# Kernel tuning notes

Hardware: AMD Instinct MI355X
Metric: run time of the kernel (lower is better)

## Reference

```python
import jax, jax.numpy as jnp
import numpy as np

NUM_CODES = 8192
LATENT_DIM = 256
BETA = 0.25
EPS_NORM = 1e-12  # F.normalize eps


def setup_inputs() -> dict:
    key = jax.random.key(0)
    k1, k2 = jax.random.split(key)
    z = jax.random.normal(k1, (8, LATENT_DIM, 32, 32), dtype=jnp.float32)
    # embedding initialized uniform(-1/K, 1/K); use that scale for realism
    codebook = jax.random.uniform(k2, (NUM_CODES, LATENT_DIM), dtype=jnp.float32,
                                  minval=-1.0 / NUM_CODES, maxval=1.0 / NUM_CODES)
    return {"z": z, "codebook": codebook}


def reference(z, codebook):
    # forward re-normalizes the codebook rows (F.normalize dim=1)
    norm = jnp.sqrt(jnp.sum(codebook * codebook, axis=1, keepdims=True))
    w = codebook / jnp.maximum(norm, EPS_NORM)                      # [K, D]

    z_perm = jnp.transpose(z, (0, 2, 3, 1))                          # [B, H, W, D]
    B, H, W, D = z_perm.shape
    zf = z_perm.reshape(-1, D)                                       # [N, D]

    # squared euclidean distances: ||z||^2 + ||w||^2 - 2 z w^T
    d = (jnp.sum(zf * zf, axis=1, keepdims=True)
         + jnp.sum(w * w, axis=1)
         - 2.0 * jnp.einsum('nd,kd->nk', zf, w))                     # [N, K]
    idx = jnp.argmin(d, axis=1)                                      # [N] int

    z_q = w[idx].reshape(B, H, W, D)                                 # gather

    # commitment + codebook loss
    loss = (jnp.mean((jax.lax.stop_gradient(z_q) - z_perm) ** 2)
            + BETA * jnp.mean((z_q - jax.lax.stop_gradient(z_perm)) ** 2))

    # straight-through estimator
    z_q = z_perm + jax.lax.stop_gradient(z_q - z_perm)

    # perplexity from codeword usage histogram (== mean of one-hots)
    N = idx.shape[0]
    counts = jnp.zeros((NUM_CODES,), dtype=jnp.float32).at[idx].add(1.0)
    avg_probs = counts / N
    perplexity = jnp.exp(-jnp.sum(avg_probs * jnp.log(avg_probs + 1e-10)))

    z_q = jnp.transpose(z_q, (0, 3, 1, 2))                           # back to NCHW
    return (z_q, idx, loss, perplexity)
```

## Files before the change

kernel.cpp:

```cpp
#include <hip/hip_runtime.h>
#include <hip/hip_bf16.h>
#include <math.h>

#define KC 8192
#define DD 256
#define NP 8192
#define ZQ_ELEMS 2097152
#define MARGIN_S 2.5e-4f
#define NPART 8

#define OFF_ABIG 0u
#define OFF_BBIG 8388608u
#define OFF_NRM  16777216u
#define OFF_WSQ  16809984u
#define OFF_PV1  16875520u
#define OFF_PV2  17924096u
#define OFF_PK1  18972672u
#define OFF_LOSSP 20021248u
#define OFF_HIST 20090880u
#define OFF_PACK 20123648u
#define OFF_LIST 20189184u
#define OFF_NFLG 20221952u

typedef __attribute__((ext_vector_type(8))) short bf16x8;
typedef __attribute__((ext_vector_type(4))) float f32x4;
typedef __attribute__((address_space(3))) void as3_void;
typedef const __attribute__((address_space(1))) void as1_cvoid;

#define GLOAD16(g, l) __builtin_amdgcn_global_load_lds((as1_cvoid*)(g), (as3_void*)(l), 16, 0, 0)

__device__ inline double waveReduceD(double v) {
#pragma unroll
    for (int off = 32; off; off >>= 1) v += __shfl_down(v, off, 64);
    return v;
}

static __device__ inline unsigned short f2bf(float f) {
    __hip_bfloat16 h = __float2bfloat16(f);
    return *(unsigned short*)&h;
}
static __device__ inline float bf2f(unsigned short u) {
    unsigned v = ((unsigned)u) << 16;
    float f;
    __builtin_memcpy(&f, &v, 4);
    return f;
}

__global__ __launch_bounds__(256) void prep(
    const float* __restrict__ cb, const float* __restrict__ z,
    unsigned short* __restrict__ Bbig, unsigned short* __restrict__ Abig,
    float* __restrict__ nrm, float* __restrict__ wsq,
    int* __restrict__ hist, int* __restrict__ nflag) {
    int bid = blockIdx.x, t = threadIdx.x;
    int lane = t & 63, wid = t >> 6;
    if (bid < 2048) {
        if (bid < 32) hist[bid * 256 + t] = 0;
        if (bid == 32 && t == 0) *nflag = 0;
        int k = bid * 4 + wid;
        float4 c4 = *(const float4*)&cb[(size_t)k * DD + lane * 4];
        double s = (double)c4.x * c4.x + (double)c4.y * c4.y
                 + (double)c4.z * c4.z + (double)c4.w * c4.w;
#pragma unroll
        for (int off = 32; off; off >>= 1) s += __shfl_xor(s, off, 64);
        float mh = fmaxf(sqrtf((float)s), 1e-12f);
        if (lane == 0) {
            nrm[k] = mh;
            wsq[k] = (float)(s / ((double)mh * (double)mh));
        }
        float wv[4] = {c4.x / mh, c4.y / mh, c4.z / mh, c4.w / mh};
        unsigned short hi[4], lo[4];
#pragma unroll
        for (int j = 0; j < 4; ++j) {
            hi[j] = f2bf(wv[j]);
            lo[j] = f2bf(wv[j] - bf2f(hi[j]));
        }
        *(ushort4*)&Bbig[(size_t)k * 512 + lane * 4] = make_ushort4(hi[0], hi[1], hi[2], hi[3]);
        *(ushort4*)&Bbig[(size_t)k * 512 + 256 + lane * 4] = make_ushort4(lo[0], lo[1], lo[2], lo[3]);
    } else {
        __shared__ float tile[64][65];
        int zb = bid - 2048;
        int b = zb >> 6, ht = (zb >> 2) & 15, dt = zb & 3;
        int hw0 = ht * 64, d0 = dt * 64;
#pragma unroll
        for (int i = 0; i < 16; ++i) {
            int dl = wid * 16 + i;
            tile[dl][lane] = z[(size_t)(b * DD + d0 + dl) * 1024 + hw0 + lane];
        }
        __syncthreads();
#pragma unroll
        for (int i = 0; i < 16; ++i) {
            int nl = wid * 16 + i;
            float v = tile[lane][nl];
            unsigned short hi = f2bf(v);
            unsigned short lo = f2bf(v - bf2f(hi));
            size_t base = (size_t)(b * 1024 + hw0 + nl) * 512 + d0 + lane;
            Abig[base] = hi;
            Abig[base + 256] = lo;
        }
    }
}

__global__ __launch_bounds__(512, 2) void gemm_top2(
    const unsigned short* __restrict__ Abig, const unsigned short* __restrict__ Bbig,
    const float* __restrict__ wsq,
    float* __restrict__ pv1, float* __restrict__ pv2, int* __restrict__ pk1) {
    __shared__ unsigned short sAB[65536];

    int t = threadIdx.x;
    int l = t & 63, w = t >> 6;
    int wm = w >> 2, wn = w & 3;
    int kc0 = blockIdx.y * 1024;
    int n0 = blockIdx.x * 256;

    int row0 = t >> 2;
    int lsw = (((t & 3) ^ ((row0 >> 1) & 3)) << 3);
    int subsw = (((l >> 4) ^ ((l >> 1) & 3)) << 3);

#define STAGE(g_) do {                                                         \
    int ct_ = (g_) / 24;                                                       \
    int kt_ = (g_) % 24;                                                       \
    int p_ = kt_ >> 3;                                                         \
    int zo_ = (p_ == 2 ? 256 : 0) + (kt_ & 7) * 32;                            \
    int wo_ = (p_ == 1 ? 256 : 0) + (kt_ & 7) * 32;                            \
    int b_ = ((g_) & 3) * 16384;                                               \
    int kc_ = kc0 + ct_ * 256;                                                 \
    GLOAD16(Bbig + (size_t)(kc_ + row0) * 512 + wo_ + lsw, &sAB[b_ + t * 8]);  \
    GLOAD16(Bbig + (size_t)(kc_ + row0 + 128) * 512 + wo_ + lsw, &sAB[b_ + 4096 + t * 8]); \
    GLOAD16(Abig + (size_t)(n0 + row0) * 512 + zo_ + lsw, &sAB[b_ + 8192 + t * 8]); \
    GLOAD16(Abig + (size_t)(n0 + row0 + 128) * 512 + zo_ + lsw, &sAB[b_ + 12288 + t * 8]); \
} while (0)

#define LDFRAG(bufbase, fa, fb) do {                                           \
    _Pragma("unroll")                                                          \
    for (int mf = 0; mf < 8; ++mf)                                             \
        fa[mf] = *(const bf16x8*)&sAB[(bufbase) + (wm * 128 + mf * 16 + (l & 15)) * 32 + subsw]; \
    _Pragma("unroll")                                                          \
    for (int nf = 0; nf < 4; ++nf)                                             \
        fb[nf] = *(const bf16x8*)&sAB[(bufbase) + 8192 + (wn * 64 + nf * 16 + (l & 15)) * 32 + subsw]; \
} while (0)

#define MFMACL(fa, fb) do {                                                    \
    __builtin_amdgcn_s_setprio(1);                                             \
    _Pragma("unroll")                                                          \
    for (int mf = 0; mf < 8; ++mf)                                             \
        _Pragma("unroll")                                                      \
        for (int nf = 0; nf < 4; ++nf)                                         \
            acc[mf][nf] = __builtin_amdgcn_mfma_f32_16x16x32_bf16(fa[mf], fb[nf], acc[mf][nf], 0, 0, 0); \
    __builtin_amdgcn_s_setprio(0);                                             \
} while (0)

#define WAITBAR(n_) do {                                                       \
    asm volatile("s_waitcnt vmcnt(" #n_ ")" ::: "memory");                     \
    __builtin_amdgcn_s_barrier();                                              \
    asm volatile("" ::: "memory");                                             \
} while (0)

#define RESETACC(ct_) do {                                                     \
    _Pragma("unroll")                                                          \
    for (int mf = 0; mf < 8; ++mf) {                                           \
        _Pragma("unroll")                                                      \
        for (int r = 0; r < 4; ++r) {                                          \
            float hv = -0.5f * wsq[kc0 + (ct_) * 256 + wm * 128 + mf * 16 + ((l >> 4) << 2) + r]; \
            _Pragma("unroll")                                                  \
            for (int nf = 0; nf < 4; ++nf) acc[mf][nf][r] = hv;                \
        }                                                                      \
    }                                                                          \
} while (0)

#define EXTRACT(ct_) do {                                                      \
    _Pragma("unroll")                                                          \
    for (int mf = 0; mf < 8; ++mf) {                                           \
        _Pragma("unroll")                                                      \
        for (int r = 0; r < 4; ++r) {                                          \
            int code = kc0 + (ct_) * 256 + wm * 128 + mf * 16 + ((l >> 4) << 2) + r; \
            _Pragma("unroll")                                                  \
            for (int nf = 0; nf < 4; ++nf) {                                   \
                float dv = -acc[mf][nf][r];                                    \
                bool lt = dv < v1[nf];                                         \
                v2[nf] = fminf(v2[nf], fmaxf(v1[nf], dv));                     \
                v1[nf] = fminf(v1[nf], dv);                                    \
                k1[nf] = lt ? code : k1[nf];                                   \
            }                                                                  \
        }                                                                      \
    }                                                                          \
} while (0)

    float v1[4], v2[4];
    int k1[4];
#pragma unroll
    for (int nf = 0; nf < 4; ++nf) { v1[nf] = 3.4e38f; v2[nf] = 3.4e38f; k1[nf] = 0; }

    f32x4 acc[8][4];
    RESETACC(0);

    bf16x8 fa0[8], fb0[4], fa1[8], fb1[4];

    STAGE(0);
    STAGE(1);
    STAGE(2);
    WAITBAR(8);
    LDFRAG(0, fa0, fb0);

    for (int g = 0; g < 94; g += 2) {
        WAITBAR(4);
        LDFRAG(((g + 1) & 3) * 16384, fa1, fb1);
        STAGE(g + 3);
        MFMACL(fa0, fb0);
        WAITBAR(4);
        LDFRAG(((g + 2) & 3) * 16384, fa0, fb0);
        if (g < 92) STAGE(g + 4);
        MFMACL(fa1, fb1);
        if (((g + 1) % 24) == 23) {
            int ct = (g + 1) / 24;
            EXTRACT(ct);
            RESETACC(ct + 1);
        }
    }
    WAITBAR(0);
    LDFRAG(3 * 16384, fa1, fb1);
    MFMACL(fa0, fb0);
    MFMACL(fa1, fb1);
    EXTRACT(3);

#pragma unroll
    for (int nf = 0; nf < 4; ++nf) {
#pragma unroll
        for (int mask = 16; mask <= 32; mask <<= 1) {
            float ov1 = __shfl_xor(v1[nf], mask, 64);
            float ov2 = __shfl_xor(v2[nf], mask, 64);
            int ok1 = __shfl_xor(k1[nf], mask, 64);
            bool take = (ov1 < v1[nf]) || (ov1 == v1[nf] && ok1 < k1[nf]);
            if (take) { v2[nf] = fminf(v1[nf], ov2); v1[nf] = ov1; k1[nf] = ok1; }
            else v2[nf] = fminf(v2[nf], ov1);
        }
    }
    __syncthreads();
    float* sv1 = (float*)sAB;
    float* sv2 = sv1 + 512;
    int* sk1 = (int*)(sv2 + 512);
    if ((l >> 4) == 0) {
#pragma unroll
        for (int nf = 0; nf < 4; ++nf) {
            int col = wn * 64 + nf * 16 + l;
            sv1[col * 2 + wm] = v1[nf];
            sv2[col * 2 + wm] = v2[nf];
            sk1[col * 2 + wm] = k1[nf];
        }
    }
    __syncthreads();
    if (t < 256) {
        float a1 = sv1[t * 2], b1 = sv1[t * 2 + 1];
        float a2 = sv2[t * 2], b2 = sv2[t * 2 + 1];
        int ak = sk1[t * 2], bk = sk1[t * 2 + 1];
        bool tb = (b1 < a1) || (b1 == a1 && bk < ak);
        float w1 = tb ? b1 : a1;
        int wk = tb ? bk : ak;
        float w2 = tb ? fminf(b2, a1) : fminf(a2, b1);
        pv1[(size_t)(n0 + t) * NPART + blockIdx.y] = w1;
        pv2[(size_t)(n0 + t) * NPART + blockIdx.y] = w2;
        pk1[(size_t)(n0 + t) * NPART + blockIdx.y] = wk;
    }
#undef STAGE
#undef LDFRAG
#undef MFMACL
#undef WAITBAR
#undef RESETACC
#undef EXTRACT
}

__global__ __launch_bounds__(256) void merge_top2(
    const float* __restrict__ pv1, const float* __restrict__ pv2,
    const int* __restrict__ pk1, int* __restrict__ list, int* __restrict__ nflag,
    unsigned long long* __restrict__ packed) {
    int n = blockIdx.x * 256 + threadIdx.x;
    float gv1 = 3.4e38f, gv2 = 3.4e38f;
    int gk1 = 0;
#pragma unroll
    for (int ct = 0; ct < NPART; ++ct) {
        float v1 = pv1[(size_t)n * NPART + ct];
        if (v1 < gv1) {
            gv2 = fminf(gv1, pv2[(size_t)n * NPART + ct]);
            gv1 = v1;
            gk1 = pk1[(size_t)n * NPART + ct];
        } else {
            gv2 = fminf(gv2, v1);
        }
    }
    int f = (gv2 - gv1 < MARGIN_S) ? 1 : 0;
    packed[n] = f ? 0xFFFFFFFFFFFFFFFFull : (unsigned long long)(unsigned)gk1;
    if (f) {
        int pos = atomicAdd(nflag, 1);
        list[pos] = n;
    }
}

__global__ __launch_bounds__(256) void rescore_par(
    const float* __restrict__ z, const float* __restrict__ cb,
    const float* __restrict__ nrm, const float* __restrict__ wsq,
    const int* __restrict__ list, const int* __restrict__ nflag,
    unsigned long long* __restrict__ packed) {
    __shared__ float sz[256];
    int nf = *nflag;
    int t = threadIdx.x;
    int lane = t & 63, wv = t >> 6;
    for (int ii = blockIdx.x; ii < nf; ii += 64) {
        int n = list[ii];
        int b = n >> 10, hw = n & 1023;
        __syncthreads();
        sz[t] = z[(b * DD + t) * 1024 + hw];
        __syncthreads();
        float4 zr = ((const float4*)sz)[lane];
        double zqd = (double)zr.x * zr.x + (double)zr.y * zr.y
                   + (double)zr.z * zr.z + (double)zr.w * zr.w;
#pragma unroll
        for (int off = 32; off; off >>= 1) zqd += __shfl_xor(zqd, off, 64);
        float zq = (float)zqd;
        unsigned long long best = 0xFFFFFFFFFFFFFFFFull;
        int kbase = blockIdx.y * 256 + wv * 64;
        for (int j = 0; j < 64; ++j) {
            int k = kbase + j;
            float4 cc = *(const float4*)&cb[(size_t)k * DD + lane * 4];
            float p = (zr.x * cc.x + zr.y * cc.y) + (zr.z * cc.z + zr.w * cc.w);
#pragma unroll
            for (int off = 32; off; off >>= 1) p += __shfl_xor(p, off, 64);
            float dot = p / nrm[k];
            float dv = (zq + wsq[k]) - 2.0f * dot;
            unsigned bits = __float_as_uint(dv);
            bits = (bits & 0x80000000u) ? ~bits : (bits | 0x80000000u);
            unsigned long long pk = ((unsigned long long)bits << 32) | (unsigned)k;
            best = best < pk ? best : pk;
        }
        if (lane == 0) atomicMin(packed + n, best);
    }
}

__global__ __launch_bounds__(256) void gather_loss(
    const float* __restrict__ z, const float* __restrict__ cb,
    const float* __restrict__ nrm, const unsigned long long* __restrict__ packed,
    float* __restrict__ out, double* __restrict__ lossp, int* __restrict__ hist) {
    __shared__ double lred[4];
    int t = threadIdx.x;
    int base = (blockIdx.x * 256 + t) * 16;
    double s = 0.0;
#pragma unroll
    for (int q = 0; q < 4; ++q) {
        int e = base + q * 4;
        int b = e >> 18, d = (e >> 10) & 255, hw = e & 1023;
        int n = (b << 10) + hw;
        float4 zv = *(const float4*)&z[e];
        float o[4];
        int ks[4];
#pragma unroll
        for (int j = 0; j < 4; ++j) {
            ks[j] = (int)(packed[n + j] & 0xFFFFFFFFull);
            o[j] = cb[ks[j] * DD + d] / nrm[ks[j]];
        }
        *(float4*)&out[e] = make_float4(o[0], o[1], o[2], o[3]);
        if (d == 0) {
#pragma unroll
            for (int j = 0; j < 4; ++j) {
                out[ZQ_ELEMS + n + j] = (float)ks[j];
                atomicAdd(&hist[ks[j]], 1);
            }
        }
        float d0 = o[0] - zv.x, d1 = o[1] - zv.y, d2 = o[2] - zv.z, d3 = o[3] - zv.w;
        s += (double)(d0 * d0) + (double)(d1 * d1) + (double)(d2 * d2) + (double)(d3 * d3);
    }
    s = waveReduceD(s);
    int lane = t & 63, wid = t >> 6;
    if (lane == 0) lred[wid] = s;
    __syncthreads();
    if (t == 0) lossp[blockIdx.x] = lred[0] + lred[1] + lred[2] + lred[3];
}

__global__ __launch_bounds__(256) void finalize_kernel(
    const int* __restrict__ hist, const double* __restrict__ lossp,
    float* __restrict__ out) {
    __shared__ double lred[4];
    __shared__ double lsum;
    int t = threadIdx.x;
    int lane = t & 63, wid = t >> 6;
    double ls = lossp[t] + lossp[t + 256];
    ls = waveReduceD(ls);
    if (lane == 0) lred[wid] = ls;
    __syncthreads();
    if (t == 0) lsum = lred[0] + lred[1] + lred[2] + lred[3];
    __syncthreads();
    double s = 0.0;
    for (int i = t; i < KC; i += 256) {
        float p = (float)hist[i] * (1.0f / 8192.0f);
        float lg = logf(p + 1e-10f);
        s += (double)(p * lg);
    }
    s = waveReduceD(s);
    if (lane == 0) lred[wid] = s;
    __syncthreads();
    if (t == 0) {
        double tot = lred[0] + lred[1] + lred[2] + lred[3];
        float m = (float)(lsum / (double)ZQ_ELEMS);
        out[ZQ_ELEMS + NP] = m + 0.25f * m;
        out[ZQ_ELEMS + NP + 1] = expf(-(float)tot);
    }
}

extern "C" void kernel_launch(void* const* d_in, const int* in_sizes, int n_in,
                              void* d_out, int out_size, void* d_ws, size_t ws_size,
                              hipStream_t stream) {
    const float* z = (const float*)d_in[0];
    const float* cb = (const float*)d_in[1];
    float* out = (float*)d_out;
    char* ws = (char*)d_ws;

    unsigned short* Abig = (unsigned short*)(ws + OFF_ABIG);
    unsigned short* Bbig = (unsigned short*)(ws + OFF_BBIG);
    float* nrm = (float*)(ws + OFF_NRM);
    float* wsq = (float*)(ws + OFF_WSQ);
    float* pv1 = (float*)(ws + OFF_PV1);
    float* pv2 = (float*)(ws + OFF_PV2);
    int* pk1 = (int*)(ws + OFF_PK1);
    int* hist = (int*)(ws + OFF_HIST);
    double* lossp = (double*)(ws + OFF_LOSSP);
    unsigned long long* packed = (unsigned long long*)(ws + OFF_PACK);
    int* list = (int*)(ws + OFF_LIST);
    int* nflag = (int*)(ws + OFF_NFLG);

    prep<<<2560, 256, 0, stream>>>(cb, z, Bbig, Abig, nrm, wsq, hist, nflag);
    gemm_top2<<<dim3(32, NPART), 512, 0, stream>>>(Abig, Bbig, wsq, pv1, pv2, pk1);
    merge_top2<<<NP / 256, 256, 0, stream>>>(pv1, pv2, pk1, list, nflag, packed);
    rescore_par<<<dim3(64, 32), 256, 0, stream>>>(z, cb, nrm, wsq, list, nflag, packed);
    gather_loss<<<ZQ_ELEMS / (256 * 16), 256, 0, stream>>>(z, cb, nrm, packed, out, lossp, hist);
    finalize_kernel<<<1, 256, 0, stream>>>(hist, lossp, out);
}
```

Before: 186.3 us.

## Replace bf16 hi/lo split GEMM with single-pass fp16 MFMA and wider margin

Drops the three-pass bf16 hi/lo split (hi*hi, hi*lo, lo*hi) for the distance GEMM and uses a single fp16 pass, so the K-loop runs a third as many iterations and the staged operands are half the size. The codebook and z are now stored as one fp16 copy each, which halves prep write traffic and GEMM load traffic. To cover the lower precision, the refinement margin grows from 2.5e-4 to 1e-2. That likely sends more candidates to the exact rescoring path, and fp16 range or precision could hurt argmin correctness if the margin is not enough.

```diff
diff --git a/kernel.cpp b/kernel.cpp
--- a/kernel.cpp
+++ b/kernel.cpp
@@ -6,23 +6,23 @@
 #define DD 256
 #define NP 8192
 #define ZQ_ELEMS 2097152
-#define MARGIN_S 2.5e-4f
+#define MARGIN_S 1e-2f
 #define NPART 8
 
 #define OFF_ABIG 0u
-#define OFF_BBIG 8388608u
-#define OFF_NRM  16777216u
-#define OFF_WSQ  16809984u
-#define OFF_PV1  16875520u
-#define OFF_PV2  17924096u
-#define OFF_PK1  18972672u
-#define OFF_LOSSP 20021248u
-#define OFF_HIST 20090880u
-#define OFF_PACK 20123648u
-#define OFF_LIST 20189184u
-#define OFF_NFLG 20221952u
-
-typedef __attribute__((ext_vector_type(8))) short bf16x8;
+#define OFF_BBIG 4194304u
+#define OFF_NRM  8388608u
+#define OFF_WSQ  8421376u
+#define OFF_PV1  8454144u
+#define OFF_PV2  8716288u
+#define OFF_PK1  8978432u
+#define OFF_LOSSP 9240576u
+#define OFF_HIST 9244672u
+#define OFF_PACK 9277440u
+#define OFF_LIST 9342976u
+#define OFF_NFLG 9375744u
+
+typedef __attribute__((ext_vector_type(8))) _Float16 f16x8;
 typedef __attribute__((ext_vector_type(4))) float f32x4;
 typedef __attribute__((address_space(3))) void as3_void;
 typedef const __attribute__((address_space(1))) void as1_cvoid;
@@ -35,15 +35,11 @@
     return v;
 }
 
-static __device__ inline unsigned short f2bf(float f) {
-    __hip_bfloat16 h = __float2bfloat16(f);
-    return *(unsigned short*)&h;
-}
-static __device__ inline float bf2f(unsigned short u) {
-    unsigned v = ((unsigned)u) << 16;
-    float f;
-    __builtin_memcpy(&f, &v, 4);
-    return f;
+static __device__ inline unsigned short f2h(float f) {
+    _Float16 h = (_Float16)f;
+    unsigned short u;
+    __builtin_memcpy(&u, &h, 2);
+    return u;
 }
 
 __global__ __launch_bounds__(256) void prep(
@@ -67,15 +63,8 @@
             nrm[k] = mh;
             wsq[k] = (float)(s / ((double)mh * (double)mh));
         }
-        float wv[4] = {c4.x / mh, c4.y / mh, c4.z / mh, c4.w / mh};
-        unsigned short hi[4], lo[4];
-#pragma unroll
-        for (int j = 0; j < 4; ++j) {
-            hi[j] = f2bf(wv[j]);
-            lo[j] = f2bf(wv[j] - bf2f(hi[j]));
-        }
-        *(ushort4*)&Bbig[(size_t)k * 512 + lane * 4] = make_ushort4(hi[0], hi[1], hi[2], hi[3]);
-        *(ushort4*)&Bbig[(size_t)k * 512 + 256 + lane * 4] = make_ushort4(lo[0], lo[1], lo[2], lo[3]);
+        *(ushort4*)&Bbig[(size_t)k * DD + lane * 4] =
+            make_ushort4(f2h(c4.x / mh), f2h(c4.y / mh), f2h(c4.z / mh), f2h(c4.w / mh));
     } else {
         __shared__ float tile[64][65];
         int zb = bid - 2048;
@@ -90,12 +79,7 @@
 #pragma unroll
         for (int i = 0; i < 16; ++i) {
             int nl = wid * 16 + i;
-            float v = tile[lane][nl];
-            unsigned short hi = f2bf(v);
-            unsigned short lo = f2bf(v - bf2f(hi));
-            size_t base = (size_t)(b * 1024 + hw0 + nl) * 512 + d0 + lane;
-            Abig[base] = hi;
-            Abig[base + 256] = lo;
+            Abig[(size_t)(b * 1024 + hw0 + nl) * DD + d0 + lane] = f2h(tile[lane][nl]);
         }
     }
 }
@@ -117,26 +101,24 @@
     int subsw = (((l >> 4) ^ ((l >> 1) & 3)) << 3);
 
 #define STAGE(g_) do {                                                         \
-    int ct_ = (g_) / 24;                                                       \
-    int kt_ = (g_) % 24;                                                       \
-    int p_ = kt_ >> 3;                                                         \
-    int zo_ = (p_ == 2 ? 256 : 0) + (kt_ & 7) * 32;                            \
-    int wo_ = (p_ == 1 ? 256 : 0) + (kt_ & 7) * 32;                            \
+    int ct_ = (g_) >> 3;                                                       \
+    int kt_ = (g_) & 7;                                                        \
+    int off_ = kt_ * 32;                                                       \
     int b_ = ((g_) & 3) * 16384;                                               \
     int kc_ = kc0 + ct_ * 256;                                                 \
-    GLOAD16(Bbig + (size_t)(kc_ + row0) * 512 + wo_ + lsw, &sAB[b_ + t * 8]);  \
-    GLOAD16(Bbig + (size_t)(kc_ + row0 + 128) * 512 + wo_ + lsw, &sAB[b_ + 4096 + t * 8]); \
-    GLOAD16(Abig + (size_t)(n0 + row0) * 512 + zo_ + lsw, &sAB[b_ + 8192 + t * 8]); \
-    GLOAD16(Abig + (size_t)(n0 + row0 + 128) * 512 + zo_ + lsw, &sAB[b_ + 12288 + t * 8]); \
+    GLOAD16(Bbig + (size_t)(kc_ + row0) * 256 + off_ + lsw, &sAB[b_ + t * 8]); \
+    GLOAD16(Bbig + (size_t)(kc_ + row0 + 128) * 256 + off_ + lsw, &sAB[b_ + 4096 + t * 8]); \
+    GLOAD16(Abig + (size_t)(n0 + row0) * 256 + off_ + lsw, &sAB[b_ + 8192 + t * 8]); \
+    GLOAD16(Abig + (size_t)(n0 + row0 + 128) * 256 + off_ + lsw, &sAB[b_ + 12288 + t * 8]); \
 } while (0)
 
 #define LDFRAG(bufbase, fa, fb) do {                                           \
     _Pragma("unroll")                                                          \
     for (int mf = 0; mf < 8; ++mf)                                             \
-        fa[mf] = *(const bf16x8*)&sAB[(bufbase) + (wm * 128 + mf * 16 + (l & 15)) * 32 + subsw]; \
+        fa[mf] = *(const f16x8*)&sAB[(bufbase) + (wm * 128 + mf * 16 + (l & 15)) * 32 + subsw]; \
     _Pragma("unroll")                                                          \
     for (int nf = 0; nf < 4; ++nf)                                             \
-        fb[nf] = *(const bf16x8*)&sAB[(bufbase) + 8192 + (wn * 64 + nf * 16 + (l & 15)) * 32 + subsw]; \
+        fb[nf] = *(const f16x8*)&sAB[(bufbase) + 8192 + (wn * 64 + nf * 16 + (l & 15)) * 32 + subsw]; \
 } while (0)
 
 #define MFMACL(fa, fb) do {                                                    \
@@ -145,7 +127,7 @@
     for (int mf = 0; mf < 8; ++mf)                                             \
         _Pragma("unroll")                                                      \
         for (int nf = 0; nf < 4; ++nf)                                         \
-            acc[mf][nf] = __builtin_amdgcn_mfma_f32_16x16x32_bf16(fa[mf], fb[nf], acc[mf][nf], 0, 0, 0); \
+            acc[mf][nf] = __builtin_amdgcn_mfma_f32_16x16x32_f16(fa[mf], fb[nf], acc[mf][nf], 0, 0, 0); \
     __builtin_amdgcn_s_setprio(0);                                             \
 } while (0)
 
@@ -193,7 +175,7 @@
     f32x4 acc[8][4];
     RESETACC(0);
 
-    bf16x8 fa0[8], fb0[4], fa1[8], fb1[4];
+    f16x8 fa0[8], fb0[4], fa1[8], fb1[4];
 
     STAGE(0);
     STAGE(1);
@@ -201,17 +183,17 @@
     WAITBAR(8);
     LDFRAG(0, fa0, fb0);
 
-    for (int g = 0; g < 94; g += 2) {
+    for (int g = 0; g < 30; g += 2) {
         WAITBAR(4);
         LDFRAG(((g + 1) & 3) * 16384, fa1, fb1);
         STAGE(g + 3);
         MFMACL(fa0, fb0);
         WAITBAR(4);
         LDFRAG(((g + 2) & 3) * 16384, fa0, fb0);
-        if (g < 92) STAGE(g + 4);
+        if (g < 28) STAGE(g + 4);
         MFMACL(fa1, fb1);
-        if (((g + 1) % 24) == 23) {
-            int ct = (g + 1) / 24;
+        if (((g + 1) & 7) == 7) {
+            int ct = (g + 1) >> 3;
             EXTRACT(ct);
             RESETACC(ct + 1);
         }
```

Result: slower. 293.1 us (median of 2 runs) (+57.3%).
